# Kernel tuning notes

Measured on AMD Instinct MI355X. Metric: run time of the kernel, lower is better.

## Reference

```python
import jax, jax.numpy as jnp
import numpy as np

B, N, DIM = 2, 4096, 1024
DEPTH, HEADS, DHEAD = 6, 8, 128
BUCKET = 64          # blindspot_size -> causal_linear_attn bucket_size
DFF = 4 * DIM
EPS_LN = 1e-5
EPS_ATTN = 1e-3


def setup_inputs() -> dict:
    key = jax.random.key(0)
    ks = jax.random.split(key, 16)
    s = 0.02
    HD = HEADS * DHEAD
    inp = {
        "x":     jax.random.normal(ks[0], (B, N, DIM), jnp.float32),
        "ln1_g": jnp.ones((DEPTH, DIM), jnp.float32),
        "ln1_b": jnp.zeros((DEPTH, DIM), jnp.float32),
        "Wq":    jax.random.normal(ks[1], (DEPTH, DIM, HD), jnp.float32) * s,
        "Wk":    jax.random.normal(ks[2], (DEPTH, DIM, HD), jnp.float32) * s,
        "Wv":    jax.random.normal(ks[3], (DEPTH, DIM, HD), jnp.float32) * s,
        "Wo":    jax.random.normal(ks[4], (DEPTH, HD, DIM), jnp.float32) * s,
        "bo":    jnp.zeros((DEPTH, DIM), jnp.float32),
        "ln2_g": jnp.ones((DEPTH, DIM), jnp.float32),
        "ln2_b": jnp.zeros((DEPTH, DIM), jnp.float32),
        "W1":    jax.random.normal(ks[5], (DEPTH, DIM, DFF), jnp.float32) * s,
        "b1":    jnp.zeros((DEPTH, DFF), jnp.float32),
        "W2":    jax.random.normal(ks[6], (DEPTH, DFF, DIM), jnp.float32) * s,
        "b2":    jnp.zeros((DEPTH, DIM), jnp.float32),
    }
    return inp


def layernorm(x, g, b):
    m = jnp.mean(x, axis=-1, keepdims=True)
    v = jnp.var(x, axis=-1, keepdims=True)
    return (x - m) * jax.lax.rsqrt(v + EPS_LN) * g + b


def causal_linear_attn(q, k, v, bucket_size=BUCKET, eps=EPS_ATTN):
    # q,k,v: [b, h, n, e]; n divisible by bucket_size. Blindspot bucketed causal linear attn.
    b, h, n, e = q.shape
    q = jax.nn.softmax(q, axis=-1) * (e ** -0.5)
    k = jnp.exp(k)
    u = n // bucket_size
    bq = q.reshape(b, h, u, bucket_size, e)
    bk = k.reshape(b, h, u, bucket_size, e)
    bv = v.reshape(b, h, u, bucket_size, e)
    b_k_cumsum = jnp.cumsum(bk.sum(axis=-2), axis=2)                     # [b,h,u,e]
    context = jnp.cumsum(jnp.einsum('bhund,bhune->bhude', bk, bv), axis=2)  # [b,h,u,e,e]
    if bucket_size > 1:
        # shift by one bucket: each bucket only sees strictly earlier buckets (blindspot)
        context = jnp.pad(context, ((0, 0), (0, 0), (1, 0), (0, 0), (0, 0)))[:, :, :-1]
        b_k_cumsum = jnp.pad(b_k_cumsum, ((0, 0), (0, 0), (1, 0), (0, 0)))[:, :, :-1]
    D_inv = 1.0 / jnp.maximum(jnp.einsum('bhud,bhund->bhun', b_k_cumsum, bq), eps)
    out = jnp.einsum('bhund,bhude,bhun->bhune', bq, context, D_inv)
    return out.reshape(b, h, n, e)


def _forward(x, ln1_g, ln1_b, Wq, Wk, Wv, Wo, bo, ln2_g, ln2_b, W1, b1, W2, b2):
    def split_heads(t):  # [b,n,h*e] -> [b,h,n,e]
        return t.reshape(B, N, HEADS, DHEAD).transpose(0, 2, 1, 3)

    def layer(x, p):
        g1, bb1_, wq, wk, wv, wo, bo_, g2, bb2_, w1, bias1, w2, bias2 = p
        h = layernorm(x, g1, bb1_)
        q, k, v = split_heads(h @ wq), split_heads(h @ wk), split_heads(h @ wv)
        a = causal_linear_attn(q, k, v)
        a = a.transpose(0, 2, 1, 3).reshape(B, N, HEADS * DHEAD)
        x = x + a @ wo + bo_
        h = layernorm(x, g2, bb2_)
        x = x + jax.nn.gelu(h @ w1 + bias1, approximate=False) @ w2 + bias2
        return x, None

    params = (ln1_g, ln1_b, Wq, Wk, Wv, Wo, bo, ln2_g, ln2_b, W1, b1, W2, b2)
    x, _ = jax.lax.scan(layer, x, params)
    return x


def reference(x, ln1_g, ln1_b, Wq, Wk, Wv, Wo, bo, ln2_g, ln2_b, W1, b1, W2, b2):
    return _forward(x, ln1_g, ln1_b, Wq, Wk, Wv, Wo, bo, ln2_g, ln2_b, W1, b1, W2, b2)
```

## Files before the change

### kernel.cpp

```cpp
#include <hip/hip_runtime.h>
#include <hip/hip_bf16.h>
#include <stdint.h>

#define TOK 8192
#define DIM 1024
#define NSEQ 4096
#define NH 8
#define DHD 128
#define NU 64
#define DFF 4096
#define NBH 16
#define QKVN 3072

typedef unsigned short u16;
typedef unsigned int u32;
typedef short bf16x8 __attribute__((ext_vector_type(8)));
typedef float f32x4 __attribute__((ext_vector_type(4)));

__device__ __forceinline__ float bu2f(u16 u) { return __uint_as_float(((u32)u) << 16); }
__device__ __forceinline__ u16 f2bu(float f) {
  union { __hip_bfloat16 b; u16 u; } cv; cv.b = __float2bfloat16(f); return cv.u;
}

typedef __attribute__((address_space(1))) void gvoid_t;
typedef __attribute__((address_space(3))) void lvoid_t;
__device__ __forceinline__ void gload16(void* lds, const void* g) {
#if __has_builtin(__builtin_amdgcn_global_load_lds)
  __builtin_amdgcn_global_load_lds((const gvoid_t*)g, (lvoid_t*)lds, 16, 0, 0);
#else
  const int l = threadIdx.x & 63;
  ((uint4*)lds)[l] = *(const uint4*)g;
#endif
}

__global__ __launch_bounds__(256) void wtrans_kernel(const float* __restrict__ W,
    u16* __restrict__ Wt, int K, int N, int dStride, int rowOff)
{
  __shared__ float T[32][33];
  const int tid = threadIdx.x;
  const size_t soff = (size_t)blockIdx.z * K * N;
  const size_t doff = (size_t)blockIdx.z * dStride;
  const int n0 = blockIdx.x << 5, k0 = blockIdx.y << 5;
  const int r = tid >> 3, c4 = (tid & 7) << 2;
  float4 v = *(const float4*)(W + soff + (size_t)(k0 + r) * N + n0 + c4);
  T[r][c4] = v.x; T[r][c4 + 1] = v.y; T[r][c4 + 2] = v.z; T[r][c4 + 3] = v.w;
  __syncthreads();
  u32 lo = (u32)f2bu(T[c4][r]) | ((u32)f2bu(T[c4 + 1][r]) << 16);
  u32 hi = (u32)f2bu(T[c4 + 2][r]) | ((u32)f2bu(T[c4 + 3][r]) << 16);
  *(uint2*)(Wt + doff + (size_t)(rowOff + n0 + r) * K + k0 + c4) = make_uint2(lo, hi);
}

__global__ __launch_bounds__(256) void ln_kernel(const float* __restrict__ x,
    const float* __restrict__ g, const float* __restrict__ bt, u16* __restrict__ h)
{
  const int row = blockIdx.x, tid = threadIdx.x;
  const int w = tid >> 6, l = tid & 63;
  float4 v = ((const float4*)(x + (size_t)row * DIM))[tid];
  float s = v.x + v.y + v.z + v.w;
  float s2 = v.x * v.x + v.y * v.y + v.z * v.z + v.w * v.w;
#pragma unroll
  for (int off = 32; off; off >>= 1) { s += __shfl_down(s, off); s2 += __shfl_down(s2, off); }
  __shared__ float ps[8];
  __shared__ float mv[2];
  if (l == 0) { ps[w] = s; ps[4 + w] = s2; }
  __syncthreads();
  if (tid == 0) {
    float S = ps[0] + ps[1] + ps[2] + ps[3];
    float S2 = ps[4] + ps[5] + ps[6] + ps[7];
    float mean = S * (1.f / 1024.f);
    float var = S2 * (1.f / 1024.f) - mean * mean;
    mv[0] = mean; mv[1] = rsqrtf(var + 1e-5f);
  }
  __syncthreads();
  const float mean = mv[0], inv = mv[1];
  const int c = tid * 4;
  float o0 = (v.x - mean) * inv * g[c + 0] + bt[c + 0];
  float o1 = (v.y - mean) * inv * g[c + 1] + bt[c + 1];
  float o2 = (v.z - mean) * inv * g[c + 2] + bt[c + 2];
  float o3 = (v.w - mean) * inv * g[c + 3] + bt[c + 3];
  u32 lo = (u32)f2bu(o0) | ((u32)f2bu(o1) << 16);
  u32 hi = (u32)f2bu(o2) | ((u32)f2bu(o3) << 16);
  ((uint2*)(h + (size_t)row * DIM))[tid] = make_uint2(lo, hi);
}

template<int DO_LN>
__global__ __launch_bounds__(256) void combine_ln_kernel(const float* __restrict__ P,
    const float* __restrict__ bias, float* __restrict__ x,
    const float* __restrict__ g, const float* __restrict__ bt, u16* __restrict__ h)
{
  const int row = blockIdx.x, tid = threadIdx.x;
  const int w = tid >> 6, l = tid & 63;
  const int c = tid * 4;
  float4 p0 = ((const float4*)(P + (size_t)row * DIM))[tid];
  float4 p1 = ((const float4*)(P + (size_t)TOK * DIM + (size_t)row * DIM))[tid];
  float4 rx = ((const float4*)(x + (size_t)row * DIM))[tid];
  float4 v;
  v.x = p0.x + p1.x + bias[c + 0] + rx.x;
  v.y = p0.y + p1.y + bias[c + 1] + rx.y;
  v.z = p0.z + p1.z + bias[c + 2] + rx.z;
  v.w = p0.w + p1.w + bias[c + 3] + rx.w;
  ((float4*)(x + (size_t)row * DIM))[tid] = v;
  if (DO_LN == 0) return;
  float s = v.x + v.y + v.z + v.w;
  float s2 = v.x * v.x + v.y * v.y + v.z * v.z + v.w * v.w;
#pragma unroll
  for (int off = 32; off; off >>= 1) { s += __shfl_down(s, off); s2 += __shfl_down(s2, off); }
  __shared__ float ps[8];
  __shared__ float mv[2];
  if (l == 0) { ps[w] = s; ps[4 + w] = s2; }
  __syncthreads();
  if (tid == 0) {
    float S = ps[0] + ps[1] + ps[2] + ps[3];
    float S2 = ps[4] + ps[5] + ps[6] + ps[7];
    float mean = S * (1.f / 1024.f);
    float var = S2 * (1.f / 1024.f) - mean * mean;
    mv[0] = mean; mv[1] = rsqrtf(var + 1e-5f);
  }
  __syncthreads();
  const float mean = mv[0], inv = mv[1];
  float o0 = (v.x - mean) * inv * g[c + 0] + bt[c + 0];
  float o1 = (v.y - mean) * inv * g[c + 1] + bt[c + 1];
  float o2 = (v.z - mean) * inv * g[c + 2] + bt[c + 2];
  float o3 = (v.w - mean) * inv * g[c + 3] + bt[c + 3];
  u32 lo = (u32)f2bu(o0) | ((u32)f2bu(o1) << 16);
  u32 hi = (u32)f2bu(o2) | ((u32)f2bu(o3) << 16);
  ((uint2*)(h + (size_t)row * DIM))[tid] = make_uint2(lo, hi);
}

template<int EPI>
__global__ __launch_bounds__(256, 2) void gemm_kernel(
    const u16* __restrict__ A, const u16* __restrict__ Bt, void* Cout,
    const float* __restrict__ bias, const float* res, u16* __restrict__ qs,
    u16* __restrict__ ket, u16* __restrict__ vt, float* __restrict__ Ksum,
    int M, int N, int K, int klen)
{
  __shared__ __align__(16) u16 As[2][128 * 32];
  __shared__ __align__(16) u16 Bs[2][128 * 32];
  __shared__ float sm[2][128];
  const int tid = threadIdx.x;
  const int w = tid >> 6, l = tid & 63;
  const int gx = gridDim.x;
  const int nwg = gx * gridDim.y;
  const int orig = blockIdx.y * gx + blockIdx.x;
  const int qq = nwg >> 3, rr = nwg & 7, xcd = orig & 7, lin = orig >> 3;
  const int wg = (xcd < rr ? xcd * (qq + 1) : rr * (qq + 1) + (xcd - rr) * qq) + lin;
  const int brow = (wg / gx) << 7, bcol = (wg % gx) << 7;
  const int wr = (w >> 1) << 6, wc = (w & 1) << 6;
  const int lr = l & 15, lk = (l >> 4) << 3;
  const int ko = (EPI == 4) ? blockIdx.z * klen : 0;
  f32x4 acc[4][4] = {};
  const int nk = klen >> 5;

#define STAGE_G(buf, kt)                                                        \
  {                                                                             \
    _Pragma("unroll")                                                           \
    for (int j = 0; j < 2; ++j) {                                               \
      int c = j * 256 + tid;                                                    \
      int rrow = c >> 2, k8 = (c & 3) << 3;                                     \
      int ub = (j * 256 + w * 64) * 8;                                          \
      gload16(&As[buf][ub], A + (size_t)(brow + rrow) * K + ko + (kt) * 32 + k8);  \
      gload16(&Bs[buf][ub], Bt + (size_t)(bcol + rrow) * K + ko + (kt) * 32 + k8); \
    }                                                                           \
  }

  STAGE_G(0, 0);
  __syncthreads();
  for (int kt = 0; kt < nk; ++kt) {
    int buf = kt & 1;
    if (kt + 1 < nk) STAGE_G(buf ^ 1, kt + 1);
    bf16x8 a[4], bb[4];
#pragma unroll
    for (int m = 0; m < 4; ++m) a[m] = *(const bf16x8*)&As[buf][(wr + m * 16 + lr) * 32 + lk];
#pragma unroll
    for (int n = 0; n < 4; ++n) bb[n] = *(const bf16x8*)&Bs[buf][(wc + n * 16 + lr) * 32 + lk];
#pragma unroll
    for (int m = 0; m < 4; ++m)
#pragma unroll
      for (int n = 0; n < 4; ++n)
        acc[m][n] = __builtin_amdgcn_mfma_f32_16x16x32_bf16(a[m], bb[n], acc[m][n], 0, 0, 0);
    __syncthreads();
  }
#undef STAGE_G
  const int l4 = (l >> 4) << 2;

  if (EPI == 3) {
    if (bcol < 1024) {
      const int wcol = w & 1;
      float rmax[4][4], rsum[4][4];
#pragma unroll
      for (int m = 0; m < 4; ++m)
#pragma unroll
        for (int r = 0; r < 4; ++r) {
          float v = fmaxf(fmaxf(acc[m][0][r], acc[m][1][r]), fmaxf(acc[m][2][r], acc[m][3][r]));
#pragma unroll
          for (int msk = 1; msk < 16; msk <<= 1) v = fmaxf(v, __shfl_xor(v, msk));
          rmax[m][r] = v;
        }
      __syncthreads();
#pragma unroll
      for (int m = 0; m < 4; ++m)
#pragma unroll
        for (int r = 0; r < 4; ++r) sm[wcol][wr + m * 16 + l4 + r] = rmax[m][r];
      __syncthreads();
#pragma unroll
      for (int m = 0; m < 4; ++m)
#pragma unroll
        for (int r = 0; r < 4; ++r) rmax[m][r] = fmaxf(rmax[m][r], sm[wcol ^ 1][wr + m * 16 + l4 + r]);
#pragma unroll
      for (int m = 0; m < 4; ++m)
#pragma unroll
        for (int r = 0; r < 4; ++r) {
          float s = 0.f;
#pragma unroll
          for (int n = 0; n < 4; ++n) {
            float e = __expf(acc[m][n][r] - rmax[m][r]);
            acc[m][n][r] = e;
            s += e;
          }
#pragma unroll
          for (int msk = 1; msk < 16; msk <<= 1) s += __shfl_xor(s, msk);
          rsum[m][r] = s;
        }
      __syncthreads();
#pragma unroll
      for (int m = 0; m < 4; ++m)
#pragma unroll
        for (int r = 0; r < 4; ++r) sm[wcol][wr + m * 16 + l4 + r] = rsum[m][r];
      __syncthreads();
#pragma unroll
      for (int m = 0; m < 4; ++m)
#pragma unroll
        for (int r = 0; r < 4; ++r) rsum[m][r] += sm[wcol ^ 1][wr + m * 16 + l4 + r];
#pragma unroll
      for (int m = 0; m < 4; ++m)
#pragma unroll
        for (int n = 0; n < 4; ++n) {
          int col = bcol + wc + n * 16 + lr;
#pragma unroll
          for (int r = 0; r < 4; ++r) {
            int row = brow + wr + m * 16 + l4 + r;
            float v = acc[m][n][r] * (0.08838834764831845f / rsum[m][r]);
            qs[(size_t)row * DIM + col] = f2bu(v);
          }
        }
    } else {
      const int isv = (bcol >= 2048);
      const int h = ((bcol - 1024) >> 7) & 7;
      const int b = brow >> 12;
      const int bh = b * 8 + h;
      const int tok0 = brow & 4095;
      u16* dst = isv ? vt : ket;
      float sums[4] = {0.f, 0.f, 0.f, 0.f};
#pragma unroll
      for (int m = 0; m < 4; ++m) {
#pragma unroll
        for (int n = 0; n < 4; ++n) {
          int e = wc + n * 16 + lr;
          int nt = tok0 + wr + m * 16 + l4;
          ushort4 pk;
          float v0 = acc[m][n][0], v1 = acc[m][n][1], v2 = acc[m][n][2], v3 = acc[m][n][3];
          if (!isv) {
            v0 = __expf(v0); v1 = __expf(v1); v2 = __expf(v2); v3 = __expf(v3);
            sums[n] += v0 + v1 + v2 + v3;
          }
          pk.x = f2bu(v0); pk.y = f2bu(v1); pk.z = f2bu(v2); pk.w = f2bu(v3);
          *(ushort4*)(dst + ((size_t)(bh * 128 + e)) * NSEQ + nt) = pk;
        }
      }
      if (!isv) {
        const int u = (tok0 + wr) >> 6;
#pragma unroll
        for (int n = 0; n < 4; ++n) {
          float s = sums[n];
          s += __shfl_xor(s, 16);
          s += __shfl_xor(s, 32);
          if ((l >> 4) == 0)
            Ksum[(((size_t)bh * 64 + u) << 7) + (wc + n * 16 + lr)] = s;
        }
      }
    }
    return;
  }

#pragma unroll
  for (int m = 0; m < 4; ++m) {
#pragma unroll
    for (int n = 0; n < 4; ++n) {
      int col = bcol + wc + n * 16 + lr;
#pragma unroll
      for (int r = 0; r < 4; ++r) {
        int row = brow + wr + m * 16 + l4 + r;
        size_t idx = (size_t)row * N + col;
        float v0 = acc[m][n][r];
        if (EPI == 1) {
          ((float*)Cout)[idx] = v0 + bias[col] + res[idx];
        } else if (EPI == 4) {
          ((float*)Cout)[(size_t)blockIdx.z * M * N + idx] = v0;
        } else {
          float t = v0 + bias[col];
          float z = 1.5957691216057308f * (t + 0.044715f * t * t * t);
          float e = __expf(z);
          float th = (e - 1.f) / (e + 1.f);
          ((u16*)Cout)[idx] = f2bu(0.5f * t * (1.f + th));
        }
      }
    }
  }
}

__global__ void kc_kernel(const float* __restrict__ Ksum, float* __restrict__ Kc)
{
  const int bh = blockIdx.x, e = threadIdx.x;
  float run = 0.f;
  for (int u = 0; u < 64; ++u) {
    size_t i = (((size_t)bh * 64 + u) << 7) + e;
    Kc[i] = run;
    run += Ksum[i];
  }
}

__global__ __launch_bounds__(256, 2) void ctx_kernel(
    const u16* __restrict__ vt, const u16* __restrict__ ket, u16* __restrict__ ctxT)
{
  __shared__ __align__(16) u16 Av[128 * 64];
  __shared__ __align__(16) u16 Bk[128 * 64];
  const int tid = threadIdx.x, w = tid >> 6, l = tid & 63;
  const int u = blockIdx.x, bh = blockIdx.y;
  const int lr = l & 15, lk = (l >> 4) << 3;
#pragma unroll
  for (int j = 0; j < 4; ++j) {
    int c = j * 256 + tid;
    int row = c >> 3, i8 = (c & 7) << 3;
    size_t goff = ((size_t)(bh * 128 + row)) * NSEQ + u * 64 + i8;
    int ub = (j * 256 + w * 64) * 8;
    gload16(&Av[ub], vt + goff);
    gload16(&Bk[ub], ket + goff);
  }
  __syncthreads();
  const int wr = (w >> 1) << 6, wc = (w & 1) << 6;
  f32x4 acc[4][4] = {};
#pragma unroll
  for (int ks = 0; ks < 2; ++ks) {
    bf16x8 a[4], bb[4];
#pragma unroll
    for (int m = 0; m < 4; ++m) a[m] = *(const bf16x8*)&Av[(wr + m * 16 + lr) * 64 + ks * 32 + lk];
#pragma unroll
    for (int n = 0; n < 4; ++n) bb[n] = *(const bf16x8*)&Bk[(wc + n * 16 + lr) * 64 + ks * 32 + lk];
#pragma unroll
    for (int m = 0; m < 4; ++m)
#pragma unroll
      for (int n = 0; n < 4; ++n)
        acc[m][n] = __builtin_amdgcn_mfma_f32_16x16x32_bf16(a[m], bb[n], acc[m][n], 0, 0, 0);
  }
  u16* out = ctxT + ((size_t)(bh * 64 + u) << 14);
  const int l4 = (l >> 4) << 2;
#pragma unroll
  for (int m = 0; m < 4; ++m)
#pragma unroll
    for (int n = 0; n < 4; ++n)
#pragma unroll
      for (int r = 0; r < 4; ++r) {
        int e = wr + m * 16 + l4 + r, d = wc + n * 16 + lr;
        out[e * 128 + d] = f2bu(acc[m][n][r]);
      }
}

__global__ void cumsum_kernel(const u16* __restrict__ ctxT, u16* __restrict__ ctxc)
{
  const size_t base = ((size_t)blockIdx.y << 20) + (size_t)blockIdx.x * 256 + threadIdx.x;
  const u16* src = ctxT + base;
  u16* dst = ctxc + base;
  float run = 0.f;
  for (int u = 0; u < 64; ++u) {
    u16 cvv = src[(size_t)u << 14];
    dst[(size_t)u << 14] = f2bu(run);
    run += bu2f(cvv);
  }
}

__global__ __launch_bounds__(256, 2) void attnout_kernel(
    const u16* __restrict__ qs, const u16* __restrict__ ctxc,
    const float* __restrict__ Kc, u16* __restrict__ aout)
{
  __shared__ __align__(16) u16 Aq[64 * 128];
  __shared__ __align__(16) u16 Bc[128 * 128];
  __shared__ float KcS[128];
  __shared__ float Dinv[64];
  const int tid = threadIdx.x, w = tid >> 6, l = tid & 63;
  const int u = blockIdx.x, bh = blockIdx.y;
  const int b = bh >> 3, h = bh & 7;
  const int lr = l & 15, lk = (l >> 4) << 3;
#pragma unroll
  for (int j = 0; j < 4; ++j) {
    int c = j * 256 + tid;
    int n = c >> 4, d8 = (c & 15) << 3;
    gload16(&Aq[(j * 256 + w * 64) * 8],
            qs + ((size_t)(b * NSEQ + u * 64 + n)) * DIM + h * 128 + d8);
  }
  const u16* csrc = ctxc + ((size_t)(bh * 64 + u) << 14);
#pragma unroll
  for (int j = 0; j < 8; ++j) {
    int c = j * 256 + tid;
    gload16(&Bc[(j * 256 + w * 64) * 8], csrc + (size_t)c * 8);
  }
  if (tid < 128) KcS[tid] = Kc[(((size_t)bh * 64 + u) << 7) + tid];
  __syncthreads();
  if (tid < 64) {
    float s = 0.f;
#pragma unroll
    for (int dd = 0; dd < 128; ++dd) {
      int d = (dd + tid * 2) & 127;
      s += bu2f(Aq[tid * 128 + d]) * KcS[d];
    }
    Dinv[tid] = 1.f / fmaxf(s, 1e-3f);
  }
  __syncthreads();
  f32x4 acc[4][2] = {};
#pragma unroll
  for (int ks = 0; ks < 4; ++ks) {
    bf16x8 a[4], bb[2];
#pragma unroll
    for (int m = 0; m < 4; ++m) a[m] = *(const bf16x8*)&Aq[(m * 16 + lr) * 128 + ks * 32 + lk];
#pragma unroll
    for (int n = 0; n < 2; ++n) bb[n] = *(const bf16x8*)&Bc[(w * 32 + n * 16 + lr) * 128 + ks * 32 + lk];
#pragma unroll
    for (int m = 0; m < 4; ++m)
#pragma unroll
      for (int n = 0; n < 2; ++n)
        acc[m][n] = __builtin_amdgcn_mfma_f32_16x16x32_bf16(a[m], bb[n], acc[m][n], 0, 0, 0);
  }
  const int l4 = (l >> 4) << 2;
#pragma unroll
  for (int m = 0; m < 4; ++m)
#pragma unroll
    for (int n = 0; n < 2; ++n)
#pragma unroll
      for (int r = 0; r < 4; ++r) {
        int nrow = m * 16 + l4 + r;
        int e = w * 32 + n * 16 + lr;
        float v = acc[m][n][r] * Dinv[nrow];
        aout[((size_t)(b * NSEQ + u * 64 + nrow)) * DIM + h * 128 + e] = f2bu(v);
      }
}

extern "C" void kernel_launch(void* const* d_in, const int* in_sizes, int n_in,
                              void* d_out, int out_size, void* d_ws, size_t ws_size,
                              hipStream_t stream)
{
  (void)in_sizes; (void)n_in; (void)out_size;
  const float* x_in = (const float*)d_in[0];
  const float* ln1g = (const float*)d_in[1];
  const float* ln1b = (const float*)d_in[2];
  const float* Wq   = (const float*)d_in[3];
  const float* Wk   = (const float*)d_in[4];
  const float* Wv   = (const float*)d_in[5];
  const float* Wo   = (const float*)d_in[6];
  const float* bo   = (const float*)d_in[7];
  const float* ln2g = (const float*)d_in[8];
  const float* ln2b = (const float*)d_in[9];
  const float* W1   = (const float*)d_in[10];
  const float* b1   = (const float*)d_in[11];
  const float* W2   = (const float*)d_in[12];
  const float* b2   = (const float*)d_in[13];
  float* x = (float*)d_out;

  char* ws = (char*)d_ws;
  size_t off = 0;
  auto alloc = [&](size_t bytes) -> char* {
    char* p = ws + off;
    off += (bytes + 255) & ~(size_t)255;
    return p;
  };
  const size_t SW = (size_t)6 * 1024 * 1024;
  const size_t BW = (size_t)6 * 4096 * 1024;
  u16* Wqkvt = (u16*)alloc(SW * 3 * 2);
  u16* Wot = (u16*)alloc(SW * 2);
  u16* W1t = (u16*)alloc(BW * 2);
  u16* W2t = (u16*)alloc(BW * 2);
  u16* hbuf = (u16*)alloc((size_t)TOK * DIM * 2);
  u16* qsb  = (u16*)alloc((size_t)TOK * DIM * 2);
  u16* ket  = (u16*)alloc((size_t)TOK * DIM * 2);
  u16* vtb  = (u16*)alloc((size_t)TOK * DIM * 2);
  u16* ab   = (u16*)alloc((size_t)TOK * DIM * 2);
  float* Ksum = (float*)alloc((size_t)NBH * 64 * 128 * 4);
  float* Kc   = (float*)alloc((size_t)NBH * 64 * 128 * 4);
  char* R = alloc((size_t)TOK * DFF * 2);
  u16* ctxT = (u16*)R;
  u16* ctxc = (u16*)(R + ((size_t)NBH * 64 * 128 * 128) * 2);
  char* midbuf = alloc((size_t)TOK * DFF * 2);
  const bool splitk = (ws_size >= off);
  u16* mid = splitk ? (u16*)midbuf : (u16*)R;
  float* P = (float*)R;

  wtrans_kernel<<<dim3(32, 32, 6), 256, 0, stream>>>(Wq, Wqkvt, 1024, 1024, QKVN * 1024, 0);
  wtrans_kernel<<<dim3(32, 32, 6), 256, 0, stream>>>(Wk, Wqkvt, 1024, 1024, QKVN * 1024, 1024);
  wtrans_kernel<<<dim3(32, 32, 6), 256, 0, stream>>>(Wv, Wqkvt, 1024, 1024, QKVN * 1024, 2048);
  wtrans_kernel<<<dim3(32, 32, 6), 256, 0, stream>>>(Wo, Wot, 1024, 1024, 1024 * 1024, 0);
  wtrans_kernel<<<dim3(128, 32, 6), 256, 0, stream>>>(W1, W1t, 1024, 4096, 4096 * 1024, 0);
  wtrans_kernel<<<dim3(32, 128, 6), 256, 0, stream>>>(W2, W2t, 4096, 1024, 4096 * 1024, 0);
  (void)hipMemcpyAsync(x, x_in, (size_t)TOK * DIM * 4, hipMemcpyDeviceToDevice, stream);

  for (int d = 0; d < 6; ++d) {
    if (d == 0 || !splitk) {
      if (d > 0)
        ln_kernel<<<TOK, 256, 0, stream>>>(x, ln1g + d * DIM, ln1b + d * DIM, hbuf);
      else
        ln_kernel<<<TOK, 256, 0, stream>>>(x, ln1g, ln1b, hbuf);
    } else {
      combine_ln_kernel<1><<<TOK, 256, 0, stream>>>(P, b2 + (d - 1) * DIM, x,
          ln1g + d * DIM, ln1b + d * DIM, hbuf);
    }
    gemm_kernel<3><<<dim3(24, 64), 256, 0, stream>>>(hbuf, Wqkvt + (size_t)d * QKVN * 1024,
        nullptr, nullptr, nullptr, qsb, ket, vtb, Ksum, TOK, QKVN, DIM, DIM);
    kc_kernel<<<NBH, 128, 0, stream>>>(Ksum, Kc);
    ctx_kernel<<<dim3(64, NBH), 256, 0, stream>>>(vtb, ket, ctxT);
    cumsum_kernel<<<dim3(64, NBH), 256, 0, stream>>>(ctxT, ctxc);
    attnout_kernel<<<dim3(64, NBH), 256, 0, stream>>>(qsb, ctxc, Kc, ab);
    gemm_kernel<1><<<dim3(8, 64), 256, 0, stream>>>(ab, Wot + (size_t)d * 1024 * 1024, x,
        bo + d * DIM, x, nullptr, nullptr, nullptr, nullptr, TOK, DIM, DIM, DIM);
    ln_kernel<<<TOK, 256, 0, stream>>>(x, ln2g + d * DIM, ln2b + d * DIM, hbuf);
    gemm_kernel<2><<<dim3(32, 64), 256, 0, stream>>>(hbuf, W1t + (size_t)d * DFF * 1024, mid,
        b1 + d * DFF, nullptr, nullptr, nullptr, nullptr, nullptr, TOK, DFF, DIM, DIM);
    if (splitk) {
      gemm_kernel<4><<<dim3(8, 64, 2), 256, 0, stream>>>(mid, W2t + (size_t)d * DFF * 1024, P,
          nullptr, nullptr, nullptr, nullptr, nullptr, nullptr, TOK, DIM, DFF, DFF / 2);
    } else {
      gemm_kernel<1><<<dim3(8, 64), 256, 0, stream>>>(mid, W2t + (size_t)d * DFF * 1024, x,
          b2 + d * DIM, x, nullptr, nullptr, nullptr, nullptr, TOK, DIM, DFF, DFF);
    }
  }
  if (splitk)
    combine_ln_kernel<0><<<TOK, 256, 0, stream>>>(P, b2 + 5 * DIM, x, nullptr, nullptr, nullptr);
}
```

Measured before the change: 2.340 ms.

## Fuse context prefix-sum, key cumsum and attention output into one streaming kernel

Replaces the key-sum prefix kernel, the context cumsum kernel and the attention output kernel with one kernel per (head, 32-column slice). Each block walks the buckets sequentially, keeping the running context prefix and key prefix in shared memory, and prefetches the next bucket's q and context rows. This removes the materialized cumulative context buffer and two launches, at the cost of far fewer blocks (64) doing serial work across 64 buckets with many barriers.

```diff
diff --git a/kernel.cpp b/kernel.cpp
--- a/kernel.cpp
+++ b/kernel.cpp
@@ -308,17 +308,6 @@
   }
 }
 
-__global__ void kc_kernel(const float* __restrict__ Ksum, float* __restrict__ Kc)
-{
-  const int bh = blockIdx.x, e = threadIdx.x;
-  float run = 0.f;
-  for (int u = 0; u < 64; ++u) {
-    size_t i = (((size_t)bh * 64 + u) << 7) + e;
-    Kc[i] = run;
-    run += Ksum[i];
-  }
-}
-
 __global__ __launch_bounds__(256, 2) void ctx_kernel(
     const u16* __restrict__ vt, const u16* __restrict__ ket, u16* __restrict__ ctxT)
 {
@@ -365,82 +354,90 @@
       }
 }
 
-__global__ void cumsum_kernel(const u16* __restrict__ ctxT, u16* __restrict__ ctxc)
-{
-  const size_t base = ((size_t)blockIdx.y << 20) + (size_t)blockIdx.x * 256 + threadIdx.x;
-  const u16* src = ctxT + base;
-  u16* dst = ctxc + base;
-  float run = 0.f;
+__global__ __launch_bounds__(256, 2) void pvfused_kernel(
+    const u16* __restrict__ qs, const u16* __restrict__ ctxT,
+    const float* __restrict__ Ksum, u16* __restrict__ aout)
+{
+  __shared__ float pf[32][128];
+  __shared__ __align__(16) u16 pb[32 * 128];
+  __shared__ float kcum[128];
+  __shared__ float DinvS[64];
+  const int tid = threadIdx.x, w = tid >> 6, l = tid & 63;
+  const int ec = blockIdx.x, bh = blockIdx.y;
+  const int b = bh >> 3, h = bh & 7;
+  const int e0 = ec << 5;
+  const int lr = l & 15, lk = (l >> 4) << 3;
+  const int te = tid >> 3, td = (tid & 7) << 4;
+  for (int i = tid; i < 32 * 128; i += 256) ((float*)pf)[i] = 0.f;
+  if (tid < 128) kcum[tid] = 0.f;
+  const u16* qbase = qs + (size_t)(b * NSEQ) * DIM + h * 128;
+  bf16x8 afc[4], afn[4], ctc[2], ctn[2];
+  float ksc = 0.f, ksn = 0.f;
+  {
+    const u16* qrow = qbase + (size_t)(w * 16 + lr) * DIM;
+#pragma unroll
+    for (int ks = 0; ks < 4; ++ks) afc[ks] = *(const bf16x8*)(qrow + ks * 32 + lk);
+    const u16* crow = ctxT + ((size_t)(bh * 64) << 14) + (e0 + te) * 128 + td;
+    ctc[0] = *(const bf16x8*)crow; ctc[1] = *(const bf16x8*)(crow + 8);
+    if (tid < 128) ksc = Ksum[(((size_t)bh * 64) << 7) + tid];
+  }
+  __syncthreads();
   for (int u = 0; u < 64; ++u) {
-    u16 cvv = src[(size_t)u << 14];
-    dst[(size_t)u << 14] = f2bu(run);
-    run += bu2f(cvv);
-  }
-}
-
-__global__ __launch_bounds__(256, 2) void attnout_kernel(
-    const u16* __restrict__ qs, const u16* __restrict__ ctxc,
-    const float* __restrict__ Kc, u16* __restrict__ aout)
-{
-  __shared__ __align__(16) u16 Aq[64 * 128];
-  __shared__ __align__(16) u16 Bc[128 * 128];
-  __shared__ float KcS[128];
-  __shared__ float Dinv[64];
-  const int tid = threadIdx.x, w = tid >> 6, l = tid & 63;
-  const int u = blockIdx.x, bh = blockIdx.y;
-  const int b = bh >> 3, h = bh & 7;
-  const int lr = l & 15, lk = (l >> 4) << 3;
-#pragma unroll
-  for (int j = 0; j < 4; ++j) {
-    int c = j * 256 + tid;
-    int n = c >> 4, d8 = (c & 15) << 3;
-    gload16(&Aq[(j * 256 + w * 64) * 8],
-            qs + ((size_t)(b * NSEQ + u * 64 + n)) * DIM + h * 128 + d8);
-  }
-  const u16* csrc = ctxc + ((size_t)(bh * 64 + u) << 14);
-#pragma unroll
-  for (int j = 0; j < 8; ++j) {
-    int c = j * 256 + tid;
-    gload16(&Bc[(j * 256 + w * 64) * 8], csrc + (size_t)c * 8);
-  }
-  if (tid < 128) KcS[tid] = Kc[(((size_t)bh * 64 + u) << 7) + tid];
-  __syncthreads();
-  if (tid < 64) {
-    float s = 0.f;
-#pragma unroll
-    for (int dd = 0; dd < 128; ++dd) {
-      int d = (dd + tid * 2) & 127;
-      s += bu2f(Aq[tid * 128 + d]) * KcS[d];
-    }
-    Dinv[tid] = 1.f / fmaxf(s, 1e-3f);
-  }
-  __syncthreads();
-  f32x4 acc[4][2] = {};
-#pragma unroll
-  for (int ks = 0; ks < 4; ++ks) {
-    bf16x8 a[4], bb[2];
-#pragma unroll
-    for (int m = 0; m < 4; ++m) a[m] = *(const bf16x8*)&Aq[(m * 16 + lr) * 128 + ks * 32 + lk];
-#pragma unroll
-    for (int n = 0; n < 2; ++n) bb[n] = *(const bf16x8*)&Bc[(w * 32 + n * 16 + lr) * 128 + ks * 32 + lk];
-#pragma unroll
-    for (int m = 0; m < 4; ++m)
-#pragma unroll
-      for (int n = 0; n < 2; ++n)
-        acc[m][n] = __builtin_amdgcn_mfma_f32_16x16x32_bf16(a[m], bb[n], acc[m][n], 0, 0, 0);
-  }
-  const int l4 = (l >> 4) << 2;
-#pragma unroll
-  for (int m = 0; m < 4; ++m)
+#pragma unroll
+    for (int j = 0; j < 16; j += 2) {
+      int d = td + j;
+      u32 pkk = (u32)f2bu(pf[te][d]) | ((u32)f2bu(pf[te][d + 1]) << 16);
+      int sb = (d * 2) ^ ((te & 15) << 4);
+      *(u32*)((char*)pb + te * 256 + sb) = pkk;
+    }
+    __syncthreads();
+    f32x4 acc[2] = {};
+    float dsum = 0.f;
+#pragma unroll
+    for (int ks = 0; ks < 4; ++ks)
+#pragma unroll
+      for (int j = 0; j < 8; ++j) dsum += bu2f((u16)afc[ks][j]) * kcum[ks * 32 + lk + j];
+    dsum += __shfl_xor(dsum, 16);
+    dsum += __shfl_xor(dsum, 32);
+    if (l < 16) DinvS[w * 16 + lr] = 1.f / fmaxf(dsum, 1e-3f);
+#pragma unroll
+    for (int n = 0; n < 2; ++n) {
+      int e = n * 16 + lr;
+#pragma unroll
+      for (int ks = 0; ks < 4; ++ks) {
+        const u16* p = (const u16*)((const char*)pb + e * 256 + (((ks * 32 + lk) * 2) ^ ((e & 15) << 4)));
+        bf16x8 bf = *(const bf16x8*)p;
+        acc[n] = __builtin_amdgcn_mfma_f32_16x16x32_bf16(afc[ks], bf, acc[n], 0, 0, 0);
+      }
+    }
+    if (u + 1 < 64) {
+      const u16* qrow = qbase + (size_t)((u + 1) * 64 + w * 16 + lr) * DIM;
+#pragma unroll
+      for (int ks = 0; ks < 4; ++ks) afn[ks] = *(const bf16x8*)(qrow + ks * 32 + lk);
+      const u16* crow = ctxT + ((size_t)(bh * 64 + u + 1) << 14) + (e0 + te) * 128 + td;
+      ctn[0] = *(const bf16x8*)crow; ctn[1] = *(const bf16x8*)(crow + 8);
+      if (tid < 128) ksn = Ksum[(((size_t)bh * 64 + u + 1) << 7) + tid];
+    }
+    __syncthreads();
+    const int l4 = (l >> 4) << 2;
 #pragma unroll
     for (int n = 0; n < 2; ++n)
 #pragma unroll
       for (int r = 0; r < 4; ++r) {
-        int nrow = m * 16 + l4 + r;
-        int e = w * 32 + n * 16 + lr;
-        float v = acc[m][n][r] * Dinv[nrow];
-        aout[((size_t)(b * NSEQ + u * 64 + nrow)) * DIM + h * 128 + e] = f2bu(v);
+        int trow = w * 16 + l4 + r;
+        float v = acc[n][r] * DinvS[trow];
+        aout[((size_t)(b * NSEQ + u * 64 + trow)) * DIM + h * 128 + e0 + n * 16 + lr] = f2bu(v);
       }
+#pragma unroll
+    for (int j = 0; j < 8; ++j) pf[te][td + j] += bu2f((u16)ctc[0][j]);
+#pragma unroll
+    for (int j = 0; j < 8; ++j) pf[te][td + 8 + j] += bu2f((u16)ctc[1][j]);
+    if (tid < 128) kcum[tid] += ksc;
+    __syncthreads();
+#pragma unroll
+    for (int ks = 0; ks < 4; ++ks) afc[ks] = afn[ks];
+    ctc[0] = ctn[0]; ctc[1] = ctn[1]; ksc = ksn;
+  }
 }
 
 extern "C" void kernel_launch(void* const* d_in, const int* in_sizes, int n_in,
@@ -483,10 +480,8 @@
   u16* vtb  = (u16*)alloc((size_t)TOK * DIM * 2);
   u16* ab   = (u16*)alloc((size_t)TOK * DIM * 2);
   float* Ksum = (float*)alloc((size_t)NBH * 64 * 128 * 4);
-  float* Kc   = (float*)alloc((size_t)NBH * 64 * 128 * 4);
   char* R = alloc((size_t)TOK * DFF * 2);
   u16* ctxT = (u16*)R;
-  u16* ctxc = (u16*)(R + ((size_t)NBH * 64 * 128 * 128) * 2);
   char* midbuf = alloc((size_t)TOK * DFF * 2);
   const bool splitk = (ws_size >= off);
   u16* mid = splitk ? (u16*)midbuf : (u16*)R;
@@ -502,20 +497,15 @@
 
   for (int d = 0; d < 6; ++d) {
     if (d == 0 || !splitk) {
-      if (d > 0)
-        ln_kernel<<<TOK, 256, 0, stream>>>(x, ln1g + d * DIM, ln1b + d * DIM, hbuf);
-      else
-        ln_kernel<<<TOK, 256, 0, stream>>>(x, ln1g, ln1b, hbuf);
+      ln_kernel<<<TOK, 256, 0, stream>>>(x, ln1g + d * DIM, ln1b + d * DIM, hbuf);
     } else {
       combine_ln_kernel<1><<<TOK, 256, 0, stream>>>(P, b2 + (d - 1) * DIM, x,
           ln1g + d * DIM, ln1b + d * DIM, hbuf);
     }
     gemm_kernel<3><<<dim3(24, 64), 256, 0, stream>>>(hbuf, Wqkvt + (size_t)d * QKVN * 1024,
         nullptr, nullptr, nullptr, qsb, ket, vtb, Ksum, TOK, QKVN, DIM, DIM);
-    kc_kernel<<<NBH, 128, 0, stream>>>(Ksum, Kc);
     ctx_kernel<<<dim3(64, NBH), 256, 0, stream>>>(vtb, ket, ctxT);
-    cumsum_kernel<<<dim3(64, NBH), 256, 0, stream>>>(ctxT, ctxc);
-    attnout_kernel<<<dim3(64, NBH), 256, 0, stream>>>(qsb, ctxc, Kc, ab);
+    pvfused_kernel<<<dim3(4, NBH), 256, 0, stream>>>(qsb, ctxT, Ksum, ab);
     gemm_kernel<1><<<dim3(8, 64), 256, 0, stream>>>(ab, Wot + (size_t)d * 1024 * 1024, x,
         bo + d * DIM, x, nullptr, nullptr, nullptr, nullptr, TOK, DIM, DIM, DIM);
     ln_kernel<<<TOK, 256, 0, stream>>>(x, ln2g + d * DIM, ln2b + d * DIM, hbuf);
```

Result: slower. 2.890 ms (+23.5%).
